# Optimization experiments

Hardware: AMD Instinct MI355X
Metric: run time of the kernel (lower is better)

Reference implementation:

```python
import jax, jax.numpy as jnp
import numpy as np

BETA = 0.25


def setup_inputs() -> dict:
    key = jax.random.key(0)
    k1, k2 = jax.random.split(key)
    z = jax.random.normal(k1, (16, 1024, 256), dtype=jnp.float32)
    embedding = jax.random.normal(k2, (8192, 256), dtype=jnp.float32)
    return {"z": z, "embedding": embedding}


def reference(z, embedding):
    e_dim = embedding.shape[-1]
    z_flat = jnp.reshape(z, (-1, e_dim))  # [N, e_dim]
    # d[i,k] = ||z_i||^2 + ||e_k||^2 - 2 z_i . e_k  -> [N, n_e]
    d = (jnp.sum(z_flat ** 2, axis=1, keepdims=True)
         + jnp.sum(embedding ** 2, axis=1)
         - 2.0 * jnp.einsum('nd,kd->nk', z_flat, embedding))
    min_encoding_indices = jnp.argmin(d, axis=1)  # [N]
    z_q = embedding[min_encoding_indices]
    z_q = jnp.reshape(z_q, z.shape)
    loss = (jnp.mean((jax.lax.stop_gradient(z_q) - z) ** 2)
            + BETA * jnp.mean((z_q - jax.lax.stop_gradient(z)) ** 2))
    z_q = z + jax.lax.stop_gradient(z_q - z)  # straight-through estimator
    return (z_q, loss, min_encoding_indices)
```

## Files before the change

### kernel.cpp

```cpp
#include <hip/hip_runtime.h>
#include <stdint.h>

#define N_ROWS   16384
#define DIM      256
#define N_CODES  8192
#define ZQ_ELEMS 4194304

typedef _Float16 f16x8 __attribute__((ext_vector_type(8)));
typedef _Float16 f16x4 __attribute__((ext_vector_type(4)));
typedef float    f32x16 __attribute__((ext_vector_type(16)));
typedef unsigned long long u64;

#define WS_ET  0
#define WS_PK  (8519680)

static __device__ __forceinline__ u64 packkey(float d, int c) {
    unsigned int u = __float_as_uint(d);
    u ^= ((unsigned int)((int)u >> 31)) | 0x80000000u;
    return ((u64)u << 32) | (unsigned int)c;
}

__global__ void vq_prep(const float* __restrict__ emb, _Float16* __restrict__ et,
                        u64* __restrict__ pkeys, float* __restrict__ loss_ptr) {
    __shared__ _Float16 sh[2][32][272];
    const int t = threadIdx.x, w = t >> 6, l = t & 63;
    if (blockIdx.x == 0 && t == 0) *loss_ptr = 0.0f;
    if (t < 64) pkeys[blockIdx.x * 64 + t] = ~0ULL;
    const int code0 = blockIdx.x * 32;
    const int sp0 = code0 >> 11, cw0 = code0 & 2047;
    #pragma unroll
    for (int j = 0; j < 8; ++j) {
        const int cl = w * 8 + j;
        float4 v = *(const float4*)(emb + (size_t)(code0 + cl) * DIM + l * 4);
        float xs[4] = {v.x, v.y, v.z, v.w};
        f16x4 hh, lo;
        float s = 0.0f;
        #pragma unroll
        for (int i = 0; i < 4; ++i) {
            _Float16 h = (_Float16)xs[i];
            hh[i] = h;
            lo[i] = (_Float16)(xs[i] - (float)h);
            s += xs[i] * xs[i];
        }
        *(f16x4*)&sh[0][cl][l * 4] = hh;
        *(f16x4*)&sh[1][cl][l * 4] = lo;
        #pragma unroll
        for (int off = 32; off > 0; off >>= 1) s += __shfl_down(s, off, 64);
        if (l == 0) {
            _Float16 nh = (_Float16)s;
            _Float16 nl = (_Float16)(s - (float)nh);
            f16x8 aug;
            #pragma unroll
            for (int i = 0; i < 8; ++i) aug[i] = (_Float16)0;
            aug[0] = nh; aug[1] = nl;
            *(f16x8*)(et + ((size_t)524288 + code0 + cl) * 8) = aug;
        }
    }
    __syncthreads();
    #pragma unroll
    for (int pp = 0; pp < 8; ++pp) {
        const int gi = pp * 256 + t;
        const int p = gi >> 10, ks = (gi >> 6) & 15, cl = (gi >> 1) & 31, h = gi & 1;
        f16x8 frag = *(const f16x8*)&sh[p][cl][ks * 16 + h * 8];
        const size_t unit = (size_t)p * 262144 + (size_t)sp0 * 65536
                          + (size_t)ks * 4096 + (size_t)(cw0 + cl) * 2 + h;
        *(f16x8*)(et + unit * 8) = frag;
    }
}

__global__ __launch_bounds__(512, 2)
void vq_main(const float* __restrict__ z, const _Float16* __restrict__ et,
             u64* __restrict__ pkeys) {
    extern __shared__ char smem[];
    u64* run = (u64*)(smem + 133120);
    float* zn = (float*)(smem + 141312);

    const int tid = threadIdx.x;
    const int w = tid >> 6, L = tid & 63, lo5 = L & 31, hi1 = L >> 5;
    const int rb = blockIdx.x >> 2, sp = blockIdx.x & 3;
    const int row0 = rb * 128, codeS = sp * 2048;

    const float* zr = z + (size_t)row0 * DIM;
    #pragma unroll
    for (int jj = 0; jj < 16; ++jj) {
        const int idx = jj * 512 + tid;
        const int r = idx >> 6, q = idx & 63;
        float4 v = *(const float4*)(zr + (size_t)r * DIM + q * 4);
        float xs[4] = {v.x, v.y, v.z, v.w};
        float ss = xs[0]*xs[0] + xs[1]*xs[1] + xs[2]*xs[2] + xs[3]*xs[3];
        f16x4 hh, lo;
        #pragma unroll
        for (int i = 0; i < 4; ++i) {
            const float m2 = -2.0f * xs[i];
            _Float16 h = (_Float16)m2;
            hh[i] = h;
            lo[i] = (_Float16)(m2 - (float)h);
        }
        char* base = smem + r * 1040 + q * 8;
        *(f16x4*)(base) = hh;
        *(f16x4*)(base + 512) = lo;
        #pragma unroll
        for (int off = 32; off > 0; off >>= 1) ss += __shfl_down(ss, off, 64);
        if (L == 0) zn[r] = ss;
    }
    run[tid] = ~0ULL;
    run[tid + 512] = ~0ULL;

    f16x8 bz;
    #pragma unroll
    for (int i = 0; i < 8; ++i) bz[i] = (_Float16)0;
    if (hi1 == 0) { bz[0] = (_Float16)1; bz[1] = (_Float16)1; }

    f32x16 zacc;
    #pragma unroll
    for (int e = 0; e < 16; ++e) zacc[e] = 0.0f;

    const f16x8* eb  = (const f16x8*)et;
    const f16x8* ebL = eb + 262144;
    const int laneU = lo5 * 2 + hi1;
    const size_t spB = (size_t)sp * 65536;
    const char* zbA = smem + (lo5 * 1040 + hi1 * 16);
    const char* zbB = zbA + 66560;

    f16x8 paug[2];
    {
        const int c0 = codeS + w * 64;
        paug[0] = eb[(size_t)524288 + c0 + lo5];
        paug[1] = eb[(size_t)524288 + c0 + 32 + lo5];
    }
    f16x8 aC0, aC1, aC2, aC3;
    {
        const size_t cu = spB + (size_t)(w * 64) * 2 + laneU;
        aC0 = eb[cu]; aC1 = eb[cu + 64]; aC2 = ebL[cu]; aC3 = ebL[cu + 64];
    }
    __syncthreads();

    for (int ci = 0; ci < 4; ++ci) {
        const int c0 = codeS + ci * 512 + w * 64;
        const size_t cu = spB + (size_t)(ci * 512 + w * 64) * 2 + laneU;
        f32x16 acc[2][4];

        __builtin_amdgcn_s_setprio(1);
        #pragma unroll
        for (int mt = 0; mt < 2; ++mt)
            #pragma unroll
            for (int nt = 0; nt < 4; ++nt)
                acc[mt][nt] = __builtin_amdgcn_mfma_f32_32x32x16_f16(paug[mt], bz, zacc, 0, 0, 0);
        __builtin_amdgcn_s_setprio(0);

        if (ci < 3) {
            const int c1 = codeS + (ci + 1) * 512 + w * 64;
            paug[0] = eb[(size_t)524288 + c1 + lo5];
            paug[1] = eb[(size_t)524288 + c1 + 32 + lo5];
        }

        #pragma unroll 4
        for (int ksg = 0; ksg < 16; ++ksg) {
            const size_t ubn = cu + (size_t)(ksg + 1) * 4096;
            f16x8 aN0 = eb[ubn], aN1 = eb[ubn + 64];
            f16x8 aN2 = ebL[ubn], aN3 = ebL[ubn + 64];

            {
                f16x8 bh0 = *(const f16x8*)(zbA + (ksg * 32));
                f16x8 bl0 = *(const f16x8*)(zbA + (ksg * 32 + 512));
                f16x8 bh1 = *(const f16x8*)(zbA + (ksg * 32 + 33280));
                f16x8 bl1 = *(const f16x8*)(zbA + (ksg * 32 + 33280 + 512));
                __builtin_amdgcn_s_setprio(1);
                acc[0][0] = __builtin_amdgcn_mfma_f32_32x32x16_f16(aC0, bh0, acc[0][0], 0, 0, 0);
                acc[0][0] = __builtin_amdgcn_mfma_f32_32x32x16_f16(aC0, bl0, acc[0][0], 0, 0, 0);
                acc[0][0] = __builtin_amdgcn_mfma_f32_32x32x16_f16(aC2, bh0, acc[0][0], 0, 0, 0);
                acc[0][1] = __builtin_amdgcn_mfma_f32_32x32x16_f16(aC0, bh1, acc[0][1], 0, 0, 0);
                acc[0][1] = __builtin_amdgcn_mfma_f32_32x32x16_f16(aC0, bl1, acc[0][1], 0, 0, 0);
                acc[0][1] = __builtin_amdgcn_mfma_f32_32x32x16_f16(aC2, bh1, acc[0][1], 0, 0, 0);
                acc[1][0] = __builtin_amdgcn_mfma_f32_32x32x16_f16(aC1, bh0, acc[1][0], 0, 0, 0);
                acc[1][0] = __builtin_amdgcn_mfma_f32_32x32x16_f16(aC1, bl0, acc[1][0], 0, 0, 0);
                acc[1][0] = __builtin_amdgcn_mfma_f32_32x32x16_f16(aC3, bh0, acc[1][0], 0, 0, 0);
                acc[1][1] = __builtin_amdgcn_mfma_f32_32x32x16_f16(aC1, bh1, acc[1][1], 0, 0, 0);
                acc[1][1] = __builtin_amdgcn_mfma_f32_32x32x16_f16(aC1, bl1, acc[1][1], 0, 0, 0);
                acc[1][1] = __builtin_amdgcn_mfma_f32_32x32x16_f16(aC3, bh1, acc[1][1], 0, 0, 0);
                __builtin_amdgcn_s_setprio(0);
            }
            {
                f16x8 bh2 = *(const f16x8*)(zbB + (ksg * 32));
                f16x8 bl2 = *(const f16x8*)(zbB + (ksg * 32 + 512));
                f16x8 bh3 = *(const f16x8*)(zbB + (ksg * 32 + 33280));
                f16x8 bl3 = *(const f16x8*)(zbB + (ksg * 32 + 33280 + 512));
                __builtin_amdgcn_s_setprio(1);
                acc[0][2] = __builtin_amdgcn_mfma_f32_32x32x16_f16(aC0, bh2, acc[0][2], 0, 0, 0);
                acc[0][2] = __builtin_amdgcn_mfma_f32_32x32x16_f16(aC0, bl2, acc[0][2], 0, 0, 0);
                acc[0][2] = __builtin_amdgcn_mfma_f32_32x32x16_f16(aC2, bh2, acc[0][2], 0, 0, 0);
                acc[0][3] = __builtin_amdgcn_mfma_f32_32x32x16_f16(aC0, bh3, acc[0][3], 0, 0, 0);
                acc[0][3] = __builtin_amdgcn_mfma_f32_32x32x16_f16(aC0, bl3, acc[0][3], 0, 0, 0);
                acc[0][3] = __builtin_amdgcn_mfma_f32_32x32x16_f16(aC2, bh3, acc[0][3], 0, 0, 0);
                acc[1][2] = __builtin_amdgcn_mfma_f32_32x32x16_f16(aC1, bh2, acc[1][2], 0, 0, 0);
                acc[1][2] = __builtin_amdgcn_mfma_f32_32x32x16_f16(aC1, bl2, acc[1][2], 0, 0, 0);
                acc[1][2] = __builtin_amdgcn_mfma_f32_32x32x16_f16(aC3, bh2, acc[1][2], 0, 0, 0);
                acc[1][3] = __builtin_amdgcn_mfma_f32_32x32x16_f16(aC1, bh3, acc[1][3], 0, 0, 0);
                acc[1][3] = __builtin_amdgcn_mfma_f32_32x32x16_f16(aC1, bl3, acc[1][3], 0, 0, 0);
                acc[1][3] = __builtin_amdgcn_mfma_f32_32x32x16_f16(aC3, bh3, acc[1][3], 0, 0, 0);
                __builtin_amdgcn_s_setprio(0);
            }
            aC0 = aN0; aC1 = aN1; aC2 = aN2; aC3 = aN3;
        }

        {
            const size_t cuN = spB + (size_t)((((ci + 1) & 3) * 512) + w * 64) * 2 + laneU;
            aC0 = eb[cuN]; aC1 = eb[cuN + 64]; aC2 = ebL[cuN]; aC3 = ebL[cuN + 64];
        }

        #pragma unroll
        for (int nt = 0; nt < 4; ++nt) {
            float mm[16];
            #pragma unroll
            for (int r = 0; r < 16; ++r)
                mm[r] = fminf(acc[0][nt][r], acc[1][nt][r]);
            #pragma unroll
            for (int s2 = 8; s2 > 0; s2 >>= 1)
                #pragma unroll
                for (int r = 0; r < 8; ++r)
                    if (r < s2) mm[r] = fminf(mm[r], mm[r + s2]);
            const float m = mm[0];
            int rel = 64;
            #pragma unroll
            for (int mt = 0; mt < 2; ++mt)
                #pragma unroll
                for (int r = 0; r < 16; ++r) {
                    const int rc = mt * 32 + (r & 3) + 8 * (r >> 2);
                    const int cand = (acc[mt][nt][r] == m) ? rc : 64;
                    rel = cand < rel ? cand : rel;
                }
            const float zrow = zn[nt * 32 + lo5];
            u64 best = packkey(m + zrow, c0 + 4 * hi1 + rel);
            const u64 o = __shfl_xor(best, 32, 64);
            if (o < best) best = o;
            if (hi1 == 0) {
                u64* p = &run[w * 128 + nt * 32 + lo5];
                if (best < *p) *p = best;
            }
        }
    }

    __syncthreads();
    if (tid < 128) {
        u64 k = run[tid];
        #pragma unroll
        for (int w2 = 1; w2 < 8; ++w2) { u64 o = run[w2 * 128 + tid]; if (o < k) k = o; }
        atomicMin(&pkeys[row0 + tid], k);
    }
}

__global__ __launch_bounds__(256)
void vq_final(const float* __restrict__ emb, const u64* __restrict__ pkeys,
              float* __restrict__ zq_out, float* __restrict__ loss_out,
              float* __restrict__ idx_out) {
    __shared__ int bestc[64];
    const int t = threadIdx.x;
    const int row0 = blockIdx.x * 64;
    if (t < 64) {
        const u64 k = pkeys[row0 + t];
        const int code = (int)(k & 0xFFFFFFFFu);
        unsigned int mu = (unsigned int)(k >> 32);
        mu = (mu & 0x80000000u) ? (mu ^ 0x80000000u) : ~mu;
        float d = __uint_as_float(mu);
        bestc[t] = code;
        idx_out[row0 + t] = (float)code;
        #pragma unroll
        for (int off = 32; off > 0; off >>= 1) d += __shfl_down(d, off, 64);
        if (t == 0) atomicAdd(loss_out, d * (1.25f / (float)ZQ_ELEMS));
    }
    __syncthreads();
    const int wave = t >> 6, lane = t & 63;
    #pragma unroll
    for (int rr = 0; rr < 16; ++rr) {
        const int rl = wave * 16 + rr;
        const int code = bestc[rl];
        float4 ev = *(const float4*)(emb + (size_t)code * DIM + lane * 4);
        *(float4*)(zq_out + (size_t)(row0 + rl) * DIM + lane * 4) = ev;
    }
}

extern "C" void kernel_launch(void* const* d_in, const int* in_sizes, int n_in,
                              void* d_out, int out_size, void* d_ws, size_t ws_size,
                              hipStream_t stream) {
    const float* z   = (const float*)d_in[0];
    const float* emb = (const float*)d_in[1];
    float* out  = (float*)d_out;
    float* zq   = out;
    float* loss = out + ZQ_ELEMS;
    float* idx  = out + ZQ_ELEMS + 1;

    char* ws = (char*)d_ws;
    _Float16* et = (_Float16*)(ws + WS_ET);
    u64*   pk    = (u64*)(ws + WS_PK);

    static bool attr_set = false;
    if (!attr_set) {
        hipFuncSetAttribute((const void*)vq_main,
                            hipFuncAttributeMaxDynamicSharedMemorySize, 141824);
        attr_set = true;
    }

    vq_prep<<<256, 256, 0, stream>>>(emb, et, pk, loss);
    vq_main<<<512, 512, 141824, stream>>>(z, et, pk);
    vq_final<<<N_ROWS / 64, 256, 0, stream>>>(emb, pk, zq, loss, idx);
}
```

Measured before the change: 253.4 us.

## Fuse final gather into main kernel via persistent grid barrier

Halves the main grid to 256 blocks, each of which now processes two row blocks in turn. The final gather/loss kernel is folded in behind a global atomic-counter barrier that spins until all 256 blocks arrive. This removes one kernel launch and its tail, and makes the grid size match 256 CUs. The cost is a spin-wait barrier that depends on all blocks being co-resident, and less parallel slack within each block.

```diff
diff --git a/kernel.cpp b/kernel.cpp
--- a/kernel.cpp
+++ b/kernel.cpp
@@ -13,6 +13,7 @@
 
 #define WS_ET  0
 #define WS_PK  (8519680)
+#define WS_CNT (8650752)
 
 static __device__ __forceinline__ u64 packkey(float d, int c) {
     unsigned int u = __float_as_uint(d);
@@ -21,10 +22,11 @@
 }
 
 __global__ void vq_prep(const float* __restrict__ emb, _Float16* __restrict__ et,
-                        u64* __restrict__ pkeys, float* __restrict__ loss_ptr) {
+                        u64* __restrict__ pkeys, unsigned int* __restrict__ cnt,
+                        float* __restrict__ loss_ptr) {
     __shared__ _Float16 sh[2][32][272];
     const int t = threadIdx.x, w = t >> 6, l = t & 63;
-    if (blockIdx.x == 0 && t == 0) *loss_ptr = 0.0f;
+    if (blockIdx.x == 0 && t == 0) { *loss_ptr = 0.0f; *cnt = 0u; }
     if (t < 64) pkeys[blockIdx.x * 64 + t] = ~0ULL;
     const int code0 = blockIdx.x * 32;
     const int sp0 = code0 >> 11, cw0 = code0 & 2047;
@@ -69,42 +71,20 @@
 }
 
 __global__ __launch_bounds__(512, 2)
-void vq_main(const float* __restrict__ z, const _Float16* __restrict__ et,
-             u64* __restrict__ pkeys) {
+void vq_main(const float* __restrict__ z, const float* __restrict__ emb,
+             const _Float16* __restrict__ et, u64* __restrict__ pkeys,
+             unsigned int* __restrict__ cnt,
+             float* __restrict__ zq_out, float* __restrict__ loss_out,
+             float* __restrict__ idx_out) {
     extern __shared__ char smem[];
     u64* run = (u64*)(smem + 133120);
+    int* bestc = (int*)(smem + 133120);
     float* zn = (float*)(smem + 141312);
 
     const int tid = threadIdx.x;
     const int w = tid >> 6, L = tid & 63, lo5 = L & 31, hi1 = L >> 5;
     const int rb = blockIdx.x >> 2, sp = blockIdx.x & 3;
-    const int row0 = rb * 128, codeS = sp * 2048;
-
-    const float* zr = z + (size_t)row0 * DIM;
-    #pragma unroll
-    for (int jj = 0; jj < 16; ++jj) {
-        const int idx = jj * 512 + tid;
-        const int r = idx >> 6, q = idx & 63;
-        float4 v = *(const float4*)(zr + (size_t)r * DIM + q * 4);
-        float xs[4] = {v.x, v.y, v.z, v.w};
-        float ss = xs[0]*xs[0] + xs[1]*xs[1] + xs[2]*xs[2] + xs[3]*xs[3];
-        f16x4 hh, lo;
-        #pragma unroll
-        for (int i = 0; i < 4; ++i) {
-            const float m2 = -2.0f * xs[i];
-            _Float16 h = (_Float16)m2;
-            hh[i] = h;
-            lo[i] = (_Float16)(m2 - (float)h);
-        }
-        char* base = smem + r * 1040 + q * 8;
-        *(f16x4*)(base) = hh;
-        *(f16x4*)(base + 512) = lo;
-        #pragma unroll
-        for (int off = 32; off > 0; off >>= 1) ss += __shfl_down(ss, off, 64);
-        if (L == 0) zn[r] = ss;
-    }
-    run[tid] = ~0ULL;
-    run[tid + 512] = ~0ULL;
+    const int codeS = sp * 2048;
 
     f16x8 bz;
     #pragma unroll
@@ -122,160 +102,193 @@
     const char* zbA = smem + (lo5 * 1040 + hi1 * 16);
     const char* zbB = zbA + 66560;
 
-    f16x8 paug[2];
-    {
-        const int c0 = codeS + w * 64;
-        paug[0] = eb[(size_t)524288 + c0 + lo5];
-        paug[1] = eb[(size_t)524288 + c0 + 32 + lo5];
-    }
-    f16x8 aC0, aC1, aC2, aC3;
-    {
-        const size_t cu = spB + (size_t)(w * 64) * 2 + laneU;
-        aC0 = eb[cu]; aC1 = eb[cu + 64]; aC2 = ebL[cu]; aC3 = ebL[cu + 64];
-    }
-    __syncthreads();
-
-    for (int ci = 0; ci < 4; ++ci) {
-        const int c0 = codeS + ci * 512 + w * 64;
-        const size_t cu = spB + (size_t)(ci * 512 + w * 64) * 2 + laneU;
-        f32x16 acc[2][4];
-
-        __builtin_amdgcn_s_setprio(1);
+    for (int pi = 0; pi < 2; ++pi) {
+        const int row0 = (rb + 64 * pi) * 128;
+        __syncthreads();
+
+        const float* zr = z + (size_t)row0 * DIM;
         #pragma unroll
-        for (int mt = 0; mt < 2; ++mt)
-            #pragma unroll
-            for (int nt = 0; nt < 4; ++nt)
-                acc[mt][nt] = __builtin_amdgcn_mfma_f32_32x32x16_f16(paug[mt], bz, zacc, 0, 0, 0);
-        __builtin_amdgcn_s_setprio(0);
-
-        if (ci < 3) {
-            const int c1 = codeS + (ci + 1) * 512 + w * 64;
-            paug[0] = eb[(size_t)524288 + c1 + lo5];
-            paug[1] = eb[(size_t)524288 + c1 + 32 + lo5];
-        }
-
-        #pragma unroll 4
-        for (int ksg = 0; ksg < 16; ++ksg) {
-            const size_t ubn = cu + (size_t)(ksg + 1) * 4096;
-            f16x8 aN0 = eb[ubn], aN1 = eb[ubn + 64];
-            f16x8 aN2 = ebL[ubn], aN3 = ebL[ubn + 64];
-
-            {
-                f16x8 bh0 = *(const f16x8*)(zbA + (ksg * 32));
-                f16x8 bl0 = *(const f16x8*)(zbA + (ksg * 32 + 512));
-                f16x8 bh1 = *(const f16x8*)(zbA + (ksg * 32 + 33280));
-                f16x8 bl1 = *(const f16x8*)(zbA + (ksg * 32 + 33280 + 512));
-                __builtin_amdgcn_s_setprio(1);
-                acc[0][0] = __builtin_amdgcn_mfma_f32_32x32x16_f16(aC0, bh0, acc[0][0], 0, 0, 0);
-                acc[0][0] = __builtin_amdgcn_mfma_f32_32x32x16_f16(aC0, bl0, acc[0][0], 0, 0, 0);
-                acc[0][0] = __builtin_amdgcn_mfma_f32_32x32x16_f16(aC2, bh0, acc[0][0], 0, 0, 0);
-                acc[0][1] = __builtin_amdgcn_mfma_f32_32x32x16_f16(aC0, bh1, acc[0][1], 0, 0, 0);
-                acc[0][1] = __builtin_amdgcn_mfma_f32_32x32x16_f16(aC0, bl1, acc[0][1], 0, 0, 0);
-                acc[0][1] = __builtin_amdgcn_mfma_f32_32x32x16_f16(aC2, bh1, acc[0][1], 0, 0, 0);
-                acc[1][0] = __builtin_amdgcn_mfma_f32_32x32x16_f16(aC1, bh0, acc[1][0], 0, 0, 0);
-                acc[1][0] = __builtin_amdgcn_mfma_f32_32x32x16_f16(aC1, bl0, acc[1][0], 0, 0, 0);
-                acc[1][0] = __builtin_amdgcn_mfma_f32_32x32x16_f16(aC3, bh0, acc[1][0], 0, 0, 0);
-                acc[1][1] = __builtin_amdgcn_mfma_f32_32x32x16_f16(aC1, bh1, acc[1][1], 0, 0, 0);
-                acc[1][1] = __builtin_amdgcn_mfma_f32_32x32x16_f16(aC1, bl1, acc[1][1], 0, 0, 0);
-                acc[1][1] = __builtin_amdgcn_mfma_f32_32x32x16_f16(aC3, bh1, acc[1][1], 0, 0, 0);
-                __builtin_amdgcn_s_setprio(0);
-            }
-            {
-                f16x8 bh2 = *(const f16x8*)(zbB + (ksg * 32));
-                f16x8 bl2 = *(const f16x8*)(zbB + (ksg * 32 + 512));
-                f16x8 bh3 = *(const f16x8*)(zbB + (ksg * 32 + 33280));
-                f16x8 bl3 = *(const f16x8*)(zbB + (ksg * 32 + 33280 + 512));
-                __builtin_amdgcn_s_setprio(1);
-                acc[0][2] = __builtin_amdgcn_mfma_f32_32x32x16_f16(aC0, bh2, acc[0][2], 0, 0, 0);
-                acc[0][2] = __builtin_amdgcn_mfma_f32_32x32x16_f16(aC0, bl2, acc[0][2], 0, 0, 0);
-                acc[0][2] = __builtin_amdgcn_mfma_f32_32x32x16_f16(aC2, bh2, acc[0][2], 0, 0, 0);
-                acc[0][3] = __builtin_amdgcn_mfma_f32_32x32x16_f16(aC0, bh3, acc[0][3], 0, 0, 0);
-                acc[0][3] = __builtin_amdgcn_mfma_f32_32x32x16_f16(aC0, bl3, acc[0][3], 0, 0, 0);
-                acc[0][3] = __builtin_amdgcn_mfma_f32_32x32x16_f16(aC2, bh3, acc[0][3], 0, 0, 0);
-                acc[1][2] = __builtin_amdgcn_mfma_f32_32x32x16_f16(aC1, bh2, acc[1][2], 0, 0, 0);
-                acc[1][2] = __builtin_amdgcn_mfma_f32_32x32x16_f16(aC1, bl2, acc[1][2], 0, 0, 0);
-                acc[1][2] = __builtin_amdgcn_mfma_f32_32x32x16_f16(aC3, bh2, acc[1][2], 0, 0, 0);
-                acc[1][3] = __builtin_amdgcn_mfma_f32_32x32x16_f16(aC1, bh3, acc[1][3], 0, 0, 0);
-                acc[1][3] = __builtin_amdgcn_mfma_f32_32x32x16_f16(aC1, bl3, acc[1][3], 0, 0, 0);
-                acc[1][3] = __builtin_amdgcn_mfma_f32_32x32x16_f16(aC3, bh3, acc[1][3], 0, 0, 0);
-                __builtin_amdgcn_s_setprio(0);
-            }
-            aC0 = aN0; aC1 = aN1; aC2 = aN2; aC3 = aN3;
-        }
-
+        for (int jj = 0; jj < 16; ++jj) {
+            const int idx = jj * 512 + tid;
+            const int r = idx >> 6, q = idx & 63;
+            float4 v = *(const float4*)(zr + (size_t)r * DIM + q * 4);
+            float xs[4] = {v.x, v.y, v.z, v.w};
+            float ss = xs[0]*xs[0] + xs[1]*xs[1] + xs[2]*xs[2] + xs[3]*xs[3];
+            f16x4 hh, lo;
+            #pragma unroll
+            for (int i = 0; i < 4; ++i) {
+                const float m2 = -2.0f * xs[i];
+                _Float16 h = (_Float16)m2;
+                hh[i] = h;
+                lo[i] = (_Float16)(m2 - (float)h);
+            }
+            char* base = smem + r * 1040 + q * 8;
+            *(f16x4*)(base) = hh;
+            *(f16x4*)(base + 512) = lo;
+            #pragma unroll
+            for (int off = 32; off > 0; off >>= 1) ss += __shfl_down(ss, off, 64);
+            if (L == 0) zn[r] = ss;
+        }
+        run[tid] = ~0ULL;
+        run[tid + 512] = ~0ULL;
+
+        f16x8 paug[2];
         {
-            const size_t cuN = spB + (size_t)((((ci + 1) & 3) * 512) + w * 64) * 2 + laneU;
-            aC0 = eb[cuN]; aC1 = eb[cuN + 64]; aC2 = ebL[cuN]; aC3 = ebL[cuN + 64];
-        }
-
-        #pragma unroll
-        for (int nt = 0; nt < 4; ++nt) {
-            float mm[16];
-            #pragma unroll
-            for (int r = 0; r < 16; ++r)
-                mm[r] = fminf(acc[0][nt][r], acc[1][nt][r]);
-            #pragma unroll
-            for (int s2 = 8; s2 > 0; s2 >>= 1)
-                #pragma unroll
-                for (int r = 0; r < 8; ++r)
-                    if (r < s2) mm[r] = fminf(mm[r], mm[r + s2]);
-            const float m = mm[0];
-            int rel = 64;
+            const int c0 = codeS + w * 64;
+            paug[0] = eb[(size_t)524288 + c0 + lo5];
+            paug[1] = eb[(size_t)524288 + c0 + 32 + lo5];
+        }
+        f16x8 aC0, aC1, aC2, aC3;
+        {
+            const size_t cu = spB + (size_t)(w * 64) * 2 + laneU;
+            aC0 = eb[cu]; aC1 = eb[cu + 64]; aC2 = ebL[cu]; aC3 = ebL[cu + 64];
+        }
+        __syncthreads();
+
+        for (int ci = 0; ci < 4; ++ci) {
+            const int c0 = codeS + ci * 512 + w * 64;
+            const size_t cu = spB + (size_t)(ci * 512 + w * 64) * 2 + laneU;
+            f32x16 acc[2][4];
+
+            __builtin_amdgcn_s_setprio(1);
             #pragma unroll
             for (int mt = 0; mt < 2; ++mt)
                 #pragma unroll
-                for (int r = 0; r < 16; ++r) {
-                    const int rc = mt * 32 + (r & 3) + 8 * (r >> 2);
-                    const int cand = (acc[mt][nt][r] == m) ? rc : 64;
-                    rel = cand < rel ? cand : rel;
+                for (int nt = 0; nt < 4; ++nt)
+                    acc[mt][nt] = __builtin_amdgcn_mfma_f32_32x32x16_f16(paug[mt], bz, zacc, 0, 0, 0);
+            __builtin_amdgcn_s_setprio(0);
+
+            if (ci < 3) {
+                const int c1 = codeS + (ci + 1) * 512 + w * 64;
+                paug[0] = eb[(size_t)524288 + c1 + lo5];
+                paug[1] = eb[(size_t)524288 + c1 + 32 + lo5];
+            }
+
+            #pragma unroll 4
+            for (int ksg = 0; ksg < 16; ++ksg) {
+                const size_t ubn = cu + (size_t)(ksg + 1) * 4096;
+                f16x8 aN0 = eb[ubn], aN1 = eb[ubn + 64];
+                f16x8 aN2 = ebL[ubn], aN3 = ebL[ubn + 64];
+
+                {
+                    f16x8 bh0 = *(const f16x8*)(zbA + (ksg * 32));
+                    f16x8 bl0 = *(const f16x8*)(zbA + (ksg * 32 + 512));
+                    f16x8 bh1 = *(const f16x8*)(zbA + (ksg * 32 + 33280));
+                    f16x8 bl1 = *(const f16x8*)(zbA + (ksg * 32 + 33280 + 512));
+                    __builtin_amdgcn_s_setprio(1);
+                    acc[0][0] = __builtin_amdgcn_mfma_f32_32x32x16_f16(aC0, bh0, acc[0][0], 0, 0, 0);
+                    acc[0][0] = __builtin_amdgcn_mfma_f32_32x32x16_f16(aC0, bl0, acc[0][0], 0, 0, 0);
+                    acc[0][0] = __builtin_amdgcn_mfma_f32_32x32x16_f16(aC2, bh0, acc[0][0], 0, 0, 0);
+                    acc[0][1] = __builtin_amdgcn_mfma_f32_32x32x16_f16(aC0, bh1, acc[0][1], 0, 0, 0);
+                    acc[0][1] = __builtin_amdgcn_mfma_f32_32x32x16_f16(aC0, bl1, acc[0][1], 0, 0, 0);
+                    acc[0][1] = __builtin_amdgcn_mfma_f32_32x32x16_f16(aC2, bh1, acc[0][1], 0, 0, 0);
+                    acc[1][0] = __builtin_amdgcn_mfma_f32_32x32x16_f16(aC1, bh0, acc[1][0], 0, 0, 0);
+                    acc[1][0] = __builtin_amdgcn_mfma_f32_32x32x16_f16(aC1, bl0, acc[1][0], 0, 0, 0);
+                    acc[1][0] = __builtin_amdgcn_mfma_f32_32x32x16_f16(aC3, bh0, acc[1][0], 0, 0, 0);
+                    acc[1][1] = __builtin_amdgcn_mfma_f32_32x32x16_f16(aC1, bh1, acc[1][1], 0, 0, 0);
+                    acc[1][1] = __builtin_amdgcn_mfma_f32_32x32x16_f16(aC1, bl1, acc[1][1], 0, 0, 0);
+                    acc[1][1] = __builtin_amdgcn_mfma_f32_32x32x16_f16(aC3, bh1, acc[1][1], 0, 0, 0);
+                    __builtin_amdgcn_s_setprio(0);
                 }
-            const float zrow = zn[nt * 32 + lo5];
-            u64 best = packkey(m + zrow, c0 + 4 * hi1 + rel);
-            const u64 o = __shfl_xor(best, 32, 64);
-            if (o < best) best = o;
-            if (hi1 == 0) {
-                u64* p = &run[w * 128 + nt * 32 + lo5];
-                if (best < *p) *p = best;
-            }
-        }
-    }
-
+                {
+                    f16x8 bh2 = *(const f16x8*)(zbB + (ksg * 32));
+                    f16x8 bl2 = *(const f16x8*)(zbB + (ksg * 32 + 512));
+                    f16x8 bh3 = *(const f16x8*)(zbB + (ksg * 32 + 33280));
+                    f16x8 bl3 = *(const f16x8*)(zbB + (ksg * 32 + 33280 + 512));
+                    __builtin_amdgcn_s_setprio(1);
+                    acc[0][2] = __builtin_amdgcn_mfma_f32_32x32x16_f16(aC0, bh2, acc[0][2], 0, 0, 0);
+                    acc[0][2] = __builtin_amdgcn_mfma_f32_32x32x16_f16(aC0, bl2, acc[0][2], 0, 0, 0);
+                    acc[0][2] = __builtin_amdgcn_mfma_f32_32x32x16_f16(aC2, bh2, acc[0][2], 0, 0, 0);
+                    acc[0][3] = __builtin_amdgcn_mfma_f32_32x32x16_f16(aC0, bh3, acc[0][3], 0, 0, 0);
+                    acc[0][3] = __builtin_amdgcn_mfma_f32_32x32x16_f16(aC0, bl3, acc[0][3], 0, 0, 0);
+                    acc[0][3] = __builtin_amdgcn_mfma_f32_32x32x16_f16(aC2, bh3, acc[0][3], 0, 0, 0);
+                    acc[1][2] = __builtin_amdgcn_mfma_f32_32x32x16_f16(aC1, bh2, acc[1][2], 0, 0, 0);
+                    acc[1][2] = __builtin_amdgcn_mfma_f32_32x32x16_f16(aC1, bl2, acc[1][2], 0, 0, 0);
+                    acc[1][2] = __builtin_amdgcn_mfma_f32_32x32x16_f16(aC3, bh2, acc[1][2], 0, 0, 0);
+                    acc[1][3] = __builtin_amdgcn_mfma_f32_32x32x16_f16(aC1, bh3, acc[1][3], 0, 0, 0);
+                    acc[1][3] = __builtin_amdgcn_mfma_f32_32x32x16_f16(aC1, bl3, acc[1][3], 0, 0, 0);
+                    acc[1][3] = __builtin_amdgcn_mfma_f32_32x32x16_f16(aC3, bh3, acc[1][3], 0, 0, 0);
+                    __builtin_amdgcn_s_setprio(0);
+                }
+                aC0 = aN0; aC1 = aN1; aC2 = aN2; aC3 = aN3;
+            }
+
+            {
+                const size_t cuN = spB + (size_t)((((ci + 1) & 3) * 512) + w * 64) * 2 + laneU;
+                aC0 = eb[cuN]; aC1 = eb[cuN + 64]; aC2 = ebL[cuN]; aC3 = ebL[cuN + 64];
+            }
+
+            #pragma unroll
+            for (int nt = 0; nt < 4; ++nt) {
+                float mm[16];
+                #pragma unroll
+                for (int r = 0; r < 16; ++r)
+                    mm[r] = fminf(acc[0][nt][r], acc[1][nt][r]);
+                #pragma unroll
+                for (int s2 = 8; s2 > 0; s2 >>= 1)
+                    #pragma unroll
+                    for (int r = 0; r < 8; ++r)
+                        if (r < s2) mm[r] = fminf(mm[r], mm[r + s2]);
+                const float m = mm[0];
+                int rel = 64;
+                #pragma unroll
+                for (int mt = 0; mt < 2; ++mt)
+                    #pragma unroll
+                    for (int r = 0; r < 16; ++r) {
+                        const int rc = mt * 32 + (r & 3) + 8 * (r >> 2);
+                        const int cand = (acc[mt][nt][r] == m) ? rc : 64;
+                        rel = cand < rel ? cand : rel;
+                    }
+                const float zrow = zn[nt * 32 + lo5];
+                u64 best = packkey(m + zrow, c0 + 4 * hi1 + rel);
+                const u64 o = __shfl_xor(best, 32, 64);
+                if (o < best) best = o;
+                if (hi1 == 0) {
+                    u64* p = &run[w * 128 + nt * 32 + lo5];
+                    if (best < *p) *p = best;
+                }
+            }
+        }
+
+        __syncthreads();
+        if (tid < 128) {
+            u64 k = run[tid];
+            #pragma unroll
+            for (int w2 = 1; w2 < 8; ++w2) { u64 o = run[w2 * 128 + tid]; if (o < k) k = o; }
+            atomicMin(&pkeys[row0 + tid], k);
+        }
+    }
+
+    asm volatile("s_waitcnt vmcnt(0)" ::: "memory");
     __syncthreads();
-    if (tid < 128) {
-        u64 k = run[tid];
+    if (tid == 0) {
+        atomicAdd(cnt, 1u);
+        while (atomicAdd(cnt, 0u) < 256u) __builtin_amdgcn_s_sleep(16);
+    }
+    __syncthreads();
+
+    {
+        const int row0f = blockIdx.x * 64;
+        if (tid < 64) {
+            const u64 k = atomicMin(&pkeys[row0f + tid], ~0ULL);
+            const int code = (int)(k & 0xFFFFFFFFu);
+            unsigned int mu = (unsigned int)(k >> 32);
+            mu = (mu & 0x80000000u) ? (mu ^ 0x80000000u) : ~mu;
+            float d = __uint_as_float(mu);
+            bestc[tid] = code;
+            idx_out[row0f + tid] = (float)code;
+            #pragma unroll
+            for (int off = 32; off > 0; off >>= 1) d += __shfl_down(d, off, 64);
+            if (tid == 0) atomicAdd(loss_out, d * (1.25f / (float)ZQ_ELEMS));
+        }
+        __syncthreads();
         #pragma unroll
-        for (int w2 = 1; w2 < 8; ++w2) { u64 o = run[w2 * 128 + tid]; if (o < k) k = o; }
-        atomicMin(&pkeys[row0 + tid], k);
-    }
-}
-
-__global__ __launch_bounds__(256)
-void vq_final(const float* __restrict__ emb, const u64* __restrict__ pkeys,
-              float* __restrict__ zq_out, float* __restrict__ loss_out,
-              float* __restrict__ idx_out) {
-    __shared__ int bestc[64];
-    const int t = threadIdx.x;
-    const int row0 = blockIdx.x * 64;
-    if (t < 64) {
-        const u64 k = pkeys[row0 + t];
-        const int code = (int)(k & 0xFFFFFFFFu);
-        unsigned int mu = (unsigned int)(k >> 32);
-        mu = (mu & 0x80000000u) ? (mu ^ 0x80000000u) : ~mu;
-        float d = __uint_as_float(mu);
-        bestc[t] = code;
-        idx_out[row0 + t] = (float)code;
-        #pragma unroll
-        for (int off = 32; off > 0; off >>= 1) d += __shfl_down(d, off, 64);
-        if (t == 0) atomicAdd(loss_out, d * (1.25f / (float)ZQ_ELEMS));
-    }
-    __syncthreads();
-    const int wave = t >> 6, lane = t & 63;
-    #pragma unroll
-    for (int rr = 0; rr < 16; ++rr) {
-        const int rl = wave * 16 + rr;
-        const int code = bestc[rl];
-        float4 ev = *(const float4*)(emb + (size_t)code * DIM + lane * 4);
-        *(float4*)(zq_out + (size_t)(row0 + rl) * DIM + lane * 4) = ev;
+        for (int rr = 0; rr < 8; ++rr) {
+            const int rl = w * 8 + rr;
+            const int code = bestc[rl];
+            float4 ev = *(const float4*)(emb + (size_t)code * DIM + L * 4);
+            *(float4*)(zq_out + (size_t)(row0f + rl) * DIM + L * 4) = ev;
+        }
     }
 }
 
@@ -292,6 +305,7 @@
     char* ws = (char*)d_ws;
     _Float16* et = (_Float16*)(ws + WS_ET);
     u64*   pk    = (u64*)(ws + WS_PK);
+    unsigned int* cn = (unsigned int*)(ws + WS_CNT);
 
     static bool attr_set = false;
     if (!attr_set) {
@@ -300,7 +314,6 @@
         attr_set = true;
     }
 
-    vq_prep<<<256, 256, 0, stream>>>(emb, et, pk, loss);
-    vq_main<<<512, 512, 141824, stream>>>(z, et, pk);
-    vq_final<<<N_ROWS / 64, 256, 0, stream>>>(emb, pk, zq, loss, idx);
+    vq_prep<<<256, 256, 0, stream>>>(emb, et, pk, cn, loss);
+    vq_main<<<256, 512, 141824, stream>>>(z, emb, et, pk, cn, zq, loss, idx);
 }
```

New measurement: 284.7 us. 12.3% more time.
